# Kernel optimization log

Measured on AMD Instinct MI355X. Metric: run time of the kernel, lower is better.

Reference implementation:

```python
import jax, jax.numpy as jnp
import numpy as np

KEEP_RATIO = 0.25
BLOCK = 8
TEMP = 0.1


def setup_inputs() -> dict:
    key = jax.random.key(0)
    features = jax.random.normal(key, (8, 256, 132, 132), dtype=jnp.float32)
    return {"features": features, "enabled": 1}


def reference(features, enabled):
    B, C, H, W = features.shape
    if not enabled:
        return jnp.ones((B, C, H, W), dtype=features.dtype)
    # pad H, W up to multiples of BLOCK (zeros, like F.pad default)
    ph = (-H) % BLOCK
    pw = (-W) % BLOCK
    x = jnp.pad(jnp.abs(features), ((0, 0), (0, 0), (0, ph), (0, pw)))
    Hp, Wp = H + ph, W + pw
    nh, nw = Hp // BLOCK, Wp // BLOCK
    # avg_pool2d(kernel=stride=BLOCK) == block-mean via reshape
    pooled = x.reshape(B, C, nh, BLOCK, nw, BLOCK).mean(axis=(3, 5))  # [B,C,nh,nw]
    total = nh * nw
    scores = pooled.reshape(B, C, total)
    keep = max(1, min(total, int(round(total * KEEP_RATIO))))
    top_vals, top_idx = jax.lax.top_k(scores, keep)  # sorted descending, like torch.topk
    # hard mask: scatter ones at topk indices
    flat_idx = top_idx.reshape(B * C, keep)
    hard = (jnp.zeros((B * C, total), dtype=features.dtype)
            .at[jnp.arange(B * C)[:, None], flat_idx].set(1.0)
            .reshape(B, C, total))
    # training-mode straight-through soft blend
    thr = jax.lax.stop_gradient(top_vals[..., -1:])  # kth value as threshold
    soft = jax.nn.sigmoid((scores - thr) / TEMP)
    soft = soft * (keep / jnp.maximum(soft.sum(-1, keepdims=True), 1e-6))
    soft = jnp.clip(soft, 0.0, 1.0)
    mask = jax.lax.stop_gradient(hard) - jax.lax.stop_gradient(soft) + soft
    # upsample blocks back to pixels (repeat_interleave) and crop padding
    block_mask = mask.reshape(B, C, nh, nw)
    full = jnp.repeat(jnp.repeat(block_mask, BLOCK, axis=2), BLOCK, axis=3)
    return full[:, :, :H, :W]
```

## Files before the change

kernel.cpp:

```cpp
#include <hip/hip_runtime.h>


#define HH 132
#define WW 132
#define NB 17
#define TOTAL 289
#define NPAD 320
#define KEEP 72
#define NTH 256
#define NC4 33
#define NCOL (17 * 33)
#define NV ((HH * WW) / 4)
#define PLANES 2048

typedef float floatx4 __attribute__((ext_vector_type(4)));

__global__ __launch_bounds__(NTH)
void gate_kernel(const float4* __restrict__ feats4,
                 const int* __restrict__ enabled_p,
                 float4* __restrict__ out4) {
    const int plane = blockIdx.x;
    const int t = threadIdx.x;
    const float4* __restrict__ fp = feats4 + (size_t)plane * NV;
    floatx4* __restrict__ op = (floatx4*)(out4 + (size_t)plane * NV);

    __shared__ __align__(16) double   s_col[NCOL];
    __shared__ __align__(16) double   s_score[NPAD];
    __shared__ __align__(16) unsigned s_key[NPAD];
    __shared__ float s_hard[TOTAL];

    for (int w = t; w < NCOL; w += NTH) {
        const int br = w / NC4;
        const int c4 = w - br * NC4;
        const int nr = (br == NB - 1) ? 4 : 8;
        const float4* cp = fp + br * (8 * NC4) + c4;
        double acc = 0.0;
        #pragma unroll
        for (int k = 0; k < 8; ++k) {
            if (k < nr) {
                const float4 x = cp[k * NC4];
                acc += (double)fabsf(x.x) + (double)fabsf(x.y)
                     + (double)fabsf(x.z) + (double)fabsf(x.w);
            }
        }
        s_col[w] = acc;
    }
    __syncthreads();

    for (int b = t; b < NPAD; b += NTH) {
        double s = 0.0;
        if (b < TOTAL) {
            const int br = b / NB;
            const int bc = b - br * NB;
            const double* rp = &s_col[br * NC4 + 2 * bc];
            s = (bc == NB - 1) ? rp[0] : (rp[0] + rp[1]);
        }
        s_score[b] = s;
        s_key[b] = (unsigned)((unsigned long long)__double_as_longlong(s) >> 32);
    }
    __syncthreads();

    const int en = *enabled_p;
    const uint4* __restrict__ sk4 = (const uint4*)s_key;
    for (int i = t; i < TOTAL; i += NTH) {
        const unsigned ki = s_key[i];
        int r = 0, e = 0;
        #pragma unroll 10
        for (int q = 0; q < NPAD / 4; ++q) {
            const uint4 k = sk4[q];
            r += (int)(k.x > ki) + (int)(k.y > ki)
               + (int)(k.z > ki) + (int)(k.w > ki);
            e += (int)(k.x == ki) + (int)(k.y == ki)
               + (int)(k.z == ki) + (int)(k.w == ki);
        }
        int rank = r;
        if (e > 1) {
            const double si = s_score[i];
            rank = 0;
            for (int j = 0; j < TOTAL; ++j) {
                const double sj = s_score[j];
                rank += (int)((sj > si) || ((sj == si) && (j < i)));
            }
        }
        s_hard[i] = (!en || rank < KEEP) ? 1.0f : 0.0f;
    }
    __syncthreads();

    for (int v = t; v < NV; v += NTH) {
        const int base = v * 4;
        const int row = base / WW;
        const int col = base - row * WW;
        const float m = s_hard[(row >> 3) * NB + (col >> 3)];
        const floatx4 mv = {m, m, m, m};
        __builtin_nontemporal_store(mv, &op[v]);
    }
}

extern "C" void kernel_launch(void* const* d_in, const int* in_sizes, int n_in,
                              void* d_out, int out_size, void* d_ws, size_t ws_size,
                              hipStream_t stream) {
    const float4* feats = (const float4*)d_in[0];
    const int* enabled = (const int*)d_in[1];
    float4* out = (float4*)d_out;
    gate_kernel<<<PLANES, NTH, 0, stream>>>(feats, enabled, out);
}
```

Before: 277.9 us.

## Stage feature plane into LDS via async global_load_lds before block pooling

Loads the whole 132x132 plane into shared memory using direct global-to-LDS loads, then computes each 8x8 block sum from LDS with rotated row order to spread bank accesses. This replaces per-column partial sums gathered straight from global memory. The aim is better load efficiency and overlap, at the cost of a much larger LDS footprint per block, which cuts occupancy.

Measured after the change: 268.5 us. 1.04x faster.

```diff
diff --git a/kernel.cpp b/kernel.cpp
--- a/kernel.cpp
+++ b/kernel.cpp
@@ -8,12 +8,13 @@
 #define NPAD 320
 #define KEEP 72
 #define NTH 256
-#define NC4 33
-#define NCOL (17 * 33)
-#define NV ((HH * WW) / 4)
+#define NV 4356
+#define NCHUNK 68
 #define PLANES 2048
 
 typedef float floatx4 __attribute__((ext_vector_type(4)));
+typedef const __attribute__((address_space(1))) void* gas_p;
+typedef __attribute__((address_space(3))) void* las_p;
 
 __global__ __launch_bounds__(NTH)
 void gate_kernel(const float4* __restrict__ feats4,
@@ -21,42 +22,58 @@
                  float4* __restrict__ out4) {
     const int plane = blockIdx.x;
     const int t = threadIdx.x;
+    const int wid = t >> 6;
+    const int lane = t & 63;
     const float4* __restrict__ fp = feats4 + (size_t)plane * NV;
-    floatx4* __restrict__ op = (floatx4*)(out4 + (size_t)plane * NV);
 
-    __shared__ __align__(16) double   s_col[NCOL];
+    __shared__ __align__(16) float4   s_plane[NV];
     __shared__ __align__(16) double   s_score[NPAD];
     __shared__ __align__(16) unsigned s_key[NPAD];
     __shared__ float s_hard[TOTAL];
 
-    for (int w = t; w < NCOL; w += NTH) {
-        const int br = w / NC4;
-        const int c4 = w - br * NC4;
-        const int nr = (br == NB - 1) ? 4 : 8;
-        const float4* cp = fp + br * (8 * NC4) + c4;
-        double acc = 0.0;
+    {
+        const int c0 = wid * 17;
         #pragma unroll
-        for (int k = 0; k < 8; ++k) {
-            if (k < nr) {
-                const float4 x = cp[k * NC4];
-                acc += (double)fabsf(x.x) + (double)fabsf(x.y)
-                     + (double)fabsf(x.z) + (double)fabsf(x.w);
-            }
+        for (int k = 0; k < 17; ++k) {
+            const int chunk = c0 + k;
+            __builtin_amdgcn_global_load_lds(
+                (gas_p)(fp + (chunk * 64 + lane)),
+                (las_p)(s_plane + chunk * 64),
+                16, 0, 0);
         }
-        s_col[w] = acc;
     }
+    if (t < NV - NCHUNK * 64)
+        s_plane[NCHUNK * 64 + t] = fp[NCHUNK * 64 + t];
     __syncthreads();
 
+    const float* __restrict__ sp = (const float*)s_plane;
     for (int b = t; b < NPAD; b += NTH) {
-        double s = 0.0;
+        double sum = 0.0;
         if (b < TOTAL) {
             const int br = b / NB;
             const int bc = b - br * NB;
-            const double* rp = &s_col[br * NC4 + 2 * bc];
-            s = (bc == NB - 1) ? rp[0] : (rp[0] + rp[1]);
+            const int nr = (br == NB - 1) ? 4 : 8;
+            const int two = (bc < NB - 1);
+            const int rot = t & 7;
+            #pragma unroll
+            for (int rr = 0; rr < 8; ++rr) {
+                const int r = (rr + rot) & 7;
+                if (r < nr) {
+                    const float* rp = sp + (br * 8 + r) * WW + bc * 8;
+                    const floatx4 a = *(const floatx4*)rp;
+                    sum += (double)fabsf(a.x) + (double)fabsf(a.y)
+                         + (double)fabsf(a.z) + (double)fabsf(a.w);
+                    if (two) {
+                        const floatx4 c = *(const floatx4*)(rp + 4);
+                        sum += (double)fabsf(c.x) + (double)fabsf(c.y)
+                             + (double)fabsf(c.z) + (double)fabsf(c.w);
+                    }
+                }
+            }
         }
-        s_score[b] = s;
-        s_key[b] = (unsigned)((unsigned long long)__double_as_longlong(s) >> 32);
+        s_score[b] = sum;
+        s_key[b] = (unsigned)((unsigned long long)
+                       __double_as_longlong(sum) >> 32);
     }
     __syncthreads();
 
@@ -86,6 +103,7 @@
     }
     __syncthreads();
 
+    floatx4* __restrict__ op = (floatx4*)(out4 + (size_t)plane * NV);
     for (int v = t; v < NV; v += NTH) {
         const int base = v * 4;
         const int row = base / WW;
```
